# Performance work log

Hardware: AMD Instinct MI355X
Metric: run time of the kernel (lower is better)

Reference implementation:

```python
import jax, jax.numpy as jnp
import numpy as np

N = 100000      # nodes
E = 1600000     # edges
G = 256         # graphs in batch
F_IN = 100      # node_features
H = 64          # hidden_channels
L = 3           # num_conv_layers


def setup_inputs() -> dict:
    key = jax.random.key(0)
    ks = jax.random.split(key, 16)
    def w(k, shape, fan_in):
        return (jax.random.normal(k, shape, jnp.float32) / np.sqrt(fan_in)).astype(jnp.float32)
    return {
        "x": jax.random.normal(ks[0], (N, F_IN), jnp.float32),
        "edge_index": jax.random.randint(ks[1], (2, E), 0, N, dtype=jnp.int32),
        "batch": jnp.sort(jax.random.randint(ks[2], (N,), 0, G, dtype=jnp.int32)),
        "W_emb": w(ks[3], (F_IN, H), F_IN),
        "b_emb": jnp.zeros((H,), jnp.float32),
        "conv_W": w(ks[4], (L, H, H), H),
        "conv_b": jnp.zeros((L, H), jnp.float32),
        "W1": w(ks[5], (H, H), H),
        "b1": jnp.zeros((H,), jnp.float32),
        "W2": w(ks[6], (H, H // 2), H),
        "b2": jnp.zeros((H // 2,), jnp.float32),
        "W3": w(ks[7], (H // 2, 1), H // 2),
        "b3": jnp.zeros((1,), jnp.float32),
    }


def reference(x, edge_index, batch, W_emb, b_emb, conv_W, conv_b, W1, b1, W2, b2, W3, b3):
    # --- GCN normalization with self-loops (PyG GCNConv defaults) ---
    loop = jnp.arange(N, dtype=edge_index.dtype)
    src = jnp.concatenate([edge_index[0], loop])  # [E+N]
    dst = jnp.concatenate([edge_index[1], loop])  # [E+N]
    deg = jax.ops.segment_sum(jnp.ones_like(dst, jnp.float32), dst, num_segments=N)
    dinv = jax.lax.rsqrt(jnp.maximum(deg, 1.0))   # deg >= 1 because of self-loops
    norm = dinv[src] * dinv[dst]                   # [E+N]

    # --- embed ---
    h = jax.nn.relu(x @ W_emb + b_emb)             # [N, H]

    # --- stacked GCNConv: h' = scatter_add(norm * (hW)[src] -> dst) + b ---
    for i in range(conv_W.shape[0]):
        hw = h @ conv_W[i]                          # [N, H]
        msg = hw[src] * norm[:, None]               # [E+N, H] gather + scale
        agg = jax.ops.segment_sum(msg, dst, num_segments=N)
        h = jax.nn.relu(agg + conv_b[i])

    # --- global mean pool over batch ids ---
    cnt = jax.ops.segment_sum(jnp.ones((N,), jnp.float32), batch, num_segments=G)
    pooled = jax.ops.segment_sum(h, batch, num_segments=G) / jnp.maximum(cnt, 1.0)[:, None]

    # --- MLP readout 64 -> 64 -> 32 -> 1 ---
    r = jax.nn.relu(pooled @ W1 + b1)
    r = jax.nn.relu(r @ W2 + b2)
    return r @ W3 + b3                              # [G, 1]
```

## Files before the change

### kernel.cpp

```cpp
#include <hip/hip_runtime.h>
#include <hip/hip_bf16.h>

#define NN 100000
#define NE 1600000
#define NG 256
#define FIN 100
#define HH 64

#define BSHIFT 9
#define BSIZE 512
#define NBUCK ((NN + BSIZE - 1) / BSIZE)
#define BCAP 9216
#define CHUNK 4096
#define NPLACE ((NE + CHUNK - 1) / CHUNK)

#define NBLK64 ((NN + 63) / 64)
#define AGG8B ((NN + 31) / 32)

#define SXE 136
#define SH 72

typedef __attribute__((ext_vector_type(8))) short short8;
typedef __attribute__((ext_vector_type(4))) float f32x4;

__device__ __forceinline__ float relu_f(float x){ return x > 0.f ? x : 0.f; }
__device__ __forceinline__ unsigned short f2b(float f) {
    unsigned int u = __float_as_uint(f);
    u += 0x7fffu + ((u >> 16) & 1u);
    return (unsigned short)(u >> 16);
}
__device__ __forceinline__ unsigned pk2(float a, float b) {
    return (unsigned)f2b(a) | ((unsigned)f2b(b) << 16);
}
__device__ __forceinline__ float b2f(unsigned short h) {
    return __uint_as_float(((unsigned int)h) << 16);
}
__device__ __forceinline__ float lo32(unsigned u){ return __uint_as_float(u << 16); }
__device__ __forceinline__ float hi32(unsigned u){ return __uint_as_float(u & 0xffff0000u); }

__global__ __launch_bounds__(256) void k_prep(const float* __restrict__ Wemb,
                                              const float* __restrict__ convW,
                                              unsigned short* __restrict__ WeT,
                                              unsigned short* __restrict__ WcT,
                                              int* __restrict__ bucket_cnt) {
    int t = threadIdx.x;
    for (int i = t; i < NBUCK; i += 256) bucket_cnt[i] = 0;
    for (int i = t; i < 64 * 128; i += 256) WeT[i] = 0;
    __syncthreads();
    for (int i = t; i < FIN * HH; i += 256) {
        int k = i >> 6, n = i & 63;
        WeT[n * 128 + k] = f2b(Wemb[i]);
    }
    for (int l = 0; l < 3; ++l)
        for (int i = t; i < HH * HH; i += 256) {
            int k = i >> 6, n = i & 63;
            WcT[l * 4096 + n * 64 + k] = f2b(convW[l * 4096 + i]);
        }
}

__global__ __launch_bounds__(256) void k_bplace(const int* __restrict__ src,
                                                const int* __restrict__ dst,
                                                int* __restrict__ bucket_cnt,
                                                unsigned int* __restrict__ upairs) {
    __shared__ int h[NBUCK];
    __shared__ int base[NBUCK];
    int t = threadIdx.x;
    for (int i = t; i < NBUCK; i += 256) h[i] = 0;
    __syncthreads();
    int e0 = blockIdx.x * CHUNK;
    int e1 = e0 + CHUNK; if (e1 > NE) e1 = NE;
    for (int i = e0 + t; i < e1; i += 256) atomicAdd(&h[dst[i] >> BSHIFT], 1);
    __syncthreads();
    for (int i = t; i < NBUCK; i += 256) {
        int c = h[i];
        base[i] = c ? atomicAdd(&bucket_cnt[i], c) : 0;
    }
    __syncthreads();
    for (int i = t; i < NBUCK; i += 256) h[i] = 0;
    __syncthreads();
    for (int i = e0 + t; i < e1; i += 256) {
        int d = dst[i];
        int b = d >> BSHIFT;
        int pos = b * BCAP + base[b] + atomicAdd(&h[b], 1);
        upairs[pos] = ((unsigned)(d & (BSIZE - 1)) << 17) | (unsigned)src[i];
    }
}

__global__ __launch_bounds__(256) void k_csr_embed(const int* __restrict__ bucket_cnt,
                                                   const unsigned int* __restrict__ upairs,
                                                   int* __restrict__ row_start,
                                                   unsigned short* __restrict__ deg16,
                                                   float* __restrict__ dinv,
                                                   int* __restrict__ csr_src,
                                                   const float* __restrict__ x,
                                                   const unsigned short* __restrict__ WeT,
                                                   const float* __restrict__ bemb,
                                                   unsigned short* __restrict__ h0) {
    __shared__ int degl[BSIZE];
    __shared__ int curl[BSIZE];
    __shared__ int wsum8[8];
    __shared__ __align__(16) unsigned short Xl[64 * SXE];
    int t = threadIdx.x;
    int lane = t & 63, w = t >> 6;

    if (blockIdx.x < NBUCK) {
        int b = blockIdx.x;
        int nbase = b << BSHIFT;
        int ncnt = NN - nbase; if (ncnt > BSIZE) ncnt = BSIZE;
        for (int i = t; i < BSIZE; i += 256) degl[i] = 0;
        __syncthreads();
        int p0 = b * BCAP;
        int p1 = p0 + bucket_cnt[b];
        for (int i = p0 + t; i < p1; i += 256) atomicAdd(&degl[upairs[i] >> 17], 1);
        __syncthreads();
        int vals[2], incs[2];
        #pragma unroll
        for (int k = 0; k < 2; ++k) {
            int seg = w + k * 4;
            int v = degl[seg * 64 + lane];
            int inc = v;
            for (int off = 1; off < 64; off <<= 1) {
                int n = __shfl_up(inc, off, 64);
                if (lane >= off) inc += n;
            }
            vals[k] = v; incs[k] = inc;
            if (lane == 63) wsum8[seg] = inc;
        }
        __syncthreads();
        #pragma unroll
        for (int k = 0; k < 2; ++k) {
            int seg = w + k * 4;
            int soff = 0;
            for (int s = 0; s < 8; ++s) if (s < seg) soff += wsum8[s];
            int idx = seg * 64 + lane;
            int rs = p0 + soff + incs[k] - vals[k];
            curl[idx] = rs;
            if (idx < ncnt) {
                row_start[nbase + idx] = rs;
                deg16[nbase + idx] = (unsigned short)vals[k];
                dinv[nbase + idx] = rsqrtf((float)(vals[k] + 1));
            }
        }
        __syncthreads();
        for (int i = p0 + t; i < p1; i += 256) {
            unsigned pk = upairs[i];
            int pos = atomicAdd(&curl[pk >> 17], 1);
            csr_src[pos] = (int)(pk & 0x1FFFFu);
        }
        return;
    }

    int row0 = (blockIdx.x - NBUCK) * 64;
    unsigned* Xl32 = (unsigned*)Xl;
    for (int i = t; i < 64 * 25; i += 256) {
        int r = i / 25, q = i - r * 25;
        int row = row0 + r;
        uint2 pkd = {0u, 0u};
        if (row < NN) {
            float4 xv = *reinterpret_cast<const float4*>(&x[(size_t)row * FIN + q * 4]);
            pkd.x = pk2(xv.x, xv.y);
            pkd.y = pk2(xv.z, xv.w);
        }
        *reinterpret_cast<uint2*>(&Xl[r * SXE + q * 4]) = pkd;
    }
    for (int i = t; i < 64 * 18; i += 256) {
        int r = i / 18, q = i - r * 18;
        Xl32[r * 68 + 50 + q] = 0u;
    }
    __syncthreads();
    int m16 = lane & 15, g4 = lane >> 4;
    f32x4 acc[4] = {{0,0,0,0},{0,0,0,0},{0,0,0,0},{0,0,0,0}};
    const unsigned short* Arow = &Xl[(w * 16 + m16) * SXE + g4 * 8];
    #pragma unroll
    for (int kk = 0; kk < 4; ++kk) {
        short8 a = *reinterpret_cast<const short8*>(Arow + kk * 32);
        #pragma unroll
        for (int c = 0; c < 4; ++c) {
            short8 bf = *reinterpret_cast<const short8*>(&WeT[(size_t)(c * 16 + m16) * 128 + g4 * 8 + kk * 32]);
            acc[c] = __builtin_amdgcn_mfma_f32_16x16x32_bf16(a, bf, acc[c], 0, 0, 0);
        }
    }
    __syncthreads();
    unsigned short* hl = Xl;
    #pragma unroll
    for (int c = 0; c < 4; ++c) {
        int col = c * 16 + m16;
        float bb = bemb[col];
        #pragma unroll
        for (int r = 0; r < 4; ++r) {
            int rr = w * 16 + g4 * 4 + r;
            hl[rr * SH + col] = f2b(relu_f(acc[c][r] + bb));
        }
    }
    __syncthreads();
    for (int i = t; i < 64 * 8; i += 256) {
        int r = i >> 3, c8 = i & 7;
        int row = row0 + r;
        if (row < NN)
            *reinterpret_cast<uint4*>(&h0[(size_t)row * HH + c8 * 8]) =
                *reinterpret_cast<const uint4*>(&hl[r * SH + c8 * 8]);
    }
}

__global__ __launch_bounds__(256) void k_gemm(const unsigned short* __restrict__ X,
                                              const unsigned short* __restrict__ WT,
                                              const float* __restrict__ dinv,
                                              unsigned short* __restrict__ gout) {
    __shared__ __align__(16) unsigned short Xl[64 * SH];
    int t = threadIdx.x, w = t >> 6, lane = t & 63;
    int row0 = blockIdx.x * 64;
    for (int i = t; i < 64 * 8; i += 256) {
        int r = i >> 3, c8 = i & 7;
        int row = row0 + r;
        short8 v = {0,0,0,0,0,0,0,0};
        if (row < NN) v = *reinterpret_cast<const short8*>(&X[(size_t)row * HH + c8 * 8]);
        *reinterpret_cast<short8*>(&Xl[r * SH + c8 * 8]) = v;
    }
    __syncthreads();
    int m16 = lane & 15, g4 = lane >> 4;
    f32x4 acc[4] = {{0,0,0,0},{0,0,0,0},{0,0,0,0},{0,0,0,0}};
    const unsigned short* Arow = &Xl[(w * 16 + m16) * SH + g4 * 8];
    #pragma unroll
    for (int kk = 0; kk < 2; ++kk) {
        short8 a = *reinterpret_cast<const short8*>(Arow + kk * 32);
        #pragma unroll
        for (int c = 0; c < 4; ++c) {
            short8 bf = *reinterpret_cast<const short8*>(&WT[(size_t)(c * 16 + m16) * 64 + g4 * 8 + kk * 32]);
            acc[c] = __builtin_amdgcn_mfma_f32_16x16x32_bf16(a, bf, acc[c], 0, 0, 0);
        }
    }
    __syncthreads();
    float dv[4];
    #pragma unroll
    for (int r = 0; r < 4; ++r) {
        int row = row0 + w * 16 + g4 * 4 + r;
        dv[r] = (row < NN) ? dinv[row] : 0.f;
    }
    #pragma unroll
    for (int c = 0; c < 4; ++c) {
        int col = c * 16 + m16;
        #pragma unroll
        for (int r = 0; r < 4; ++r) {
            int rr = w * 16 + g4 * 4 + r;
            Xl[rr * SH + col] = f2b(dv[r] * acc[c][r]);
        }
    }
    __syncthreads();
    for (int i = t; i < 64 * 8; i += 256) {
        int r = i >> 3, c8 = i & 7;
        int row = row0 + r;
        if (row < NN)
            *reinterpret_cast<uint4*>(&gout[(size_t)row * HH + c8 * 8]) =
                *reinterpret_cast<const uint4*>(&Xl[r * SH + c8 * 8]);
    }
}

__global__ __launch_bounds__(256) void k_agg8(const int* __restrict__ row_start,
                                              const unsigned short* __restrict__ deg16,
                                              const int* __restrict__ csr_src,
                                              const unsigned short* __restrict__ g,
                                              const float* __restrict__ dinv,
                                              const float* __restrict__ bL,
                                              unsigned short* __restrict__ hout) {
    int t = threadIdx.x;
    int lane = t & 63, w = t >> 6;
    int oct = lane >> 3;
    int sub = lane & 7;
    int v = (blockIdx.x * 4 + w) * 8 + oct;
    bool valid = v < NN;
    int st = 0, n = 0;
    float a0=0.f,a1=0.f,a2=0.f,a3=0.f,a4=0.f,a5=0.f,a6=0.f,a7=0.f;
    if (valid) {
        st = row_start[v];
        n = deg16[v];
        uint4 u = *reinterpret_cast<const uint4*>(&g[(size_t)v * HH + sub * 8]);
        a0 = lo32(u.x); a1 = hi32(u.x); a2 = lo32(u.y); a3 = hi32(u.y);
        a4 = lo32(u.z); a5 = hi32(u.z); a6 = lo32(u.w); a7 = hi32(u.w);
    }
    int sb = oct << 3;
    for (int base = 0; base < n; base += 8) {
        int m = n - base; if (m > 8) m = 8;
        int sv = (sub < m) ? csr_src[st + base + sub] : 0;
        int j = 0;
        for (; j + 4 <= m; j += 4) {
            int s0 = __shfl(sv, sb + j),     s1 = __shfl(sv, sb + j + 1);
            int s2 = __shfl(sv, sb + j + 2), s3 = __shfl(sv, sb + j + 3);
            uint4 u0 = *reinterpret_cast<const uint4*>(&g[(size_t)s0 * HH + sub * 8]);
            uint4 u1 = *reinterpret_cast<const uint4*>(&g[(size_t)s1 * HH + sub * 8]);
            uint4 u2 = *reinterpret_cast<const uint4*>(&g[(size_t)s2 * HH + sub * 8]);
            uint4 u3 = *reinterpret_cast<const uint4*>(&g[(size_t)s3 * HH + sub * 8]);
            a0 += lo32(u0.x); a1 += hi32(u0.x); a2 += lo32(u0.y); a3 += hi32(u0.y);
            a4 += lo32(u0.z); a5 += hi32(u0.z); a6 += lo32(u0.w); a7 += hi32(u0.w);
            a0 += lo32(u1.x); a1 += hi32(u1.x); a2 += lo32(u1.y); a3 += hi32(u1.y);
            a4 += lo32(u1.z); a5 += hi32(u1.z); a6 += lo32(u1.w); a7 += hi32(u1.w);
            a0 += lo32(u2.x); a1 += hi32(u2.x); a2 += lo32(u2.y); a3 += hi32(u2.y);
            a4 += lo32(u2.z); a5 += hi32(u2.z); a6 += lo32(u2.w); a7 += hi32(u2.w);
            a0 += lo32(u3.x); a1 += hi32(u3.x); a2 += lo32(u3.y); a3 += hi32(u3.y);
            a4 += lo32(u3.z); a5 += hi32(u3.z); a6 += lo32(u3.w); a7 += hi32(u3.w);
        }
        for (; j < m; ++j) {
            int s = __shfl(sv, sb + j);
            uint4 u = *reinterpret_cast<const uint4*>(&g[(size_t)s * HH + sub * 8]);
            a0 += lo32(u.x); a1 += hi32(u.x); a2 += lo32(u.y); a3 += hi32(u.y);
            a4 += lo32(u.z); a5 += hi32(u.z); a6 += lo32(u.w); a7 += hi32(u.w);
        }
    }
    if (valid) {
        float4 bb0 = *reinterpret_cast<const float4*>(&bL[sub * 8]);
        float4 bb1 = *reinterpret_cast<const float4*>(&bL[sub * 8 + 4]);
        float dv = dinv[v];
        uint4 outv;
        outv.x = pk2(relu_f(dv * a0 + bb0.x), relu_f(dv * a1 + bb0.y));
        outv.y = pk2(relu_f(dv * a2 + bb0.z), relu_f(dv * a3 + bb0.w));
        outv.z = pk2(relu_f(dv * a4 + bb1.x), relu_f(dv * a5 + bb1.y));
        outv.w = pk2(relu_f(dv * a6 + bb1.z), relu_f(dv * a7 + bb1.w));
        *reinterpret_cast<uint4*>(&hout[(size_t)v * HH + sub * 8]) = outv;
    }
}

__global__ __launch_bounds__(512) void k_pool_mlp(const unsigned short* __restrict__ h,
                                                  const int* __restrict__ batch,
                                                  const float* __restrict__ W1, const float* __restrict__ b1,
                                                  const float* __restrict__ W2, const float* __restrict__ b2,
                                                  const float* __restrict__ W3, const float* __restrict__ b3,
                                                  float* __restrict__ out) {
    int g = blockIdx.x;
    int lo = 0, hi_s = NN;
    while (lo < hi_s) { int mid = (lo + hi_s) >> 1; if (batch[mid] < g) lo = mid + 1; else hi_s = mid; }
    int lo2 = lo, hi = NN;
    while (lo2 < hi) { int mid = (lo2 + hi) >> 1; if (batch[mid] < g + 1) lo2 = mid + 1; else hi = mid; }
    int lane = threadIdx.x & 63;
    int wave = threadIdx.x >> 6;
    float s = 0.f;
    for (int n = lo + wave; n < hi; n += 8) {
        s += b2f(h[(size_t)n * HH + lane]);
    }
    __shared__ float red[8][64];
    __shared__ float pv[64];
    __shared__ float tv[64];
    __shared__ float qv[32];
    red[wave][lane] = s;
    __syncthreads();
    int cnt = hi - lo;
    float invc = 1.f / (float)(cnt > 0 ? cnt : 1);
    if (threadIdx.x < 64) {
        float acc = 0.f;
        #pragma unroll
        for (int r = 0; r < 8; ++r) acc += red[r][lane];
        pv[lane] = acc * invc;
    }
    __syncthreads();
    if (threadIdx.x < 64) {
        int j = threadIdx.x;
        float s1 = b1[j];
        #pragma unroll
        for (int k = 0; k < 64; ++k) s1 = fmaf(pv[k], W1[k * 64 + j], s1);
        tv[j] = relu_f(s1);
    }
    __syncthreads();
    if (threadIdx.x < 32) {
        int j = threadIdx.x;
        float s2 = b2[j];
        #pragma unroll
        for (int k = 0; k < 64; ++k) s2 = fmaf(tv[k], W2[k * 32 + j], s2);
        qv[j] = relu_f(s2);
    }
    __syncthreads();
    if (threadIdx.x == 0) {
        float s3 = b3[0];
        #pragma unroll
        for (int k = 0; k < 32; ++k) s3 = fmaf(qv[k], W3[k], s3);
        out[g] = s3;
    }
}

extern "C" void kernel_launch(void* const* d_in, const int* in_sizes, int n_in,
                              void* d_out, int out_size, void* d_ws, size_t ws_size,
                              hipStream_t stream) {
    const float* x    = (const float*)d_in[0];
    const int*   ei   = (const int*)d_in[1];
    const int*   batch= (const int*)d_in[2];
    const float* Wemb = (const float*)d_in[3];
    const float* bemb = (const float*)d_in[4];
    const float* convW= (const float*)d_in[5];
    const float* convb= (const float*)d_in[6];
    const float* W1   = (const float*)d_in[7];
    const float* b1   = (const float*)d_in[8];
    const float* W2   = (const float*)d_in[9];
    const float* b2   = (const float*)d_in[10];
    const float* W3   = (const float*)d_in[11];
    const float* b3   = (const float*)d_in[12];
    float* out = (float*)d_out;

    auto alignup = [](size_t v) { return (v + 255) & ~(size_t)255; };
    char* p = (char*)d_ws;
    int*   row_start    = (int*)p;            p += alignup((size_t)NN * 4);
    unsigned short* deg16 = (unsigned short*)p; p += alignup((size_t)NN * 2);
    float* dinv         = (float*)p;          p += alignup((size_t)NN * 4);
    int*   bucket_cnt   = (int*)p;            p += alignup((size_t)NBUCK * 4);
    int*   csr_src      = (int*)p;            p += alignup((size_t)NBUCK * BCAP * 4);
    unsigned short* WeT = (unsigned short*)p; p += alignup((size_t)64 * 128 * 2);
    unsigned short* WcT = (unsigned short*)p; p += alignup((size_t)3 * 4096 * 2);
    unsigned short* hbuf = (unsigned short*)p; p += alignup((size_t)NN * HH * 2);
    unsigned short* gbuf = (unsigned short*)p; p += alignup((size_t)NN * HH * 2);
    unsigned int* upairs = (unsigned int*)gbuf;

    const int* srcA = ei;
    const int* dstA = ei + NE;

    k_prep<<<1, 256, 0, stream>>>(Wemb, convW, WeT, WcT, bucket_cnt);
    k_bplace<<<NPLACE, 256, 0, stream>>>(srcA, dstA, bucket_cnt, upairs);

    k_csr_embed<<<NBUCK + NBLK64, 256, 0, stream>>>(bucket_cnt, upairs, row_start, deg16, dinv,
                                                    csr_src, x, WeT, bemb, hbuf);

    k_gemm<<<NBLK64, 256, 0, stream>>>(hbuf, WcT + 0 * 4096, dinv, gbuf);
    k_agg8<<<AGG8B, 256, 0, stream>>>(row_start, deg16, csr_src, gbuf, dinv, convb + 0 * HH, hbuf);
    k_gemm<<<NBLK64, 256, 0, stream>>>(hbuf, WcT + 1 * 4096, dinv, gbuf);
    k_agg8<<<AGG8B, 256, 0, stream>>>(row_start, deg16, csr_src, gbuf, dinv, convb + 1 * HH, hbuf);
    k_gemm<<<NBLK64, 256, 0, stream>>>(hbuf, WcT + 2 * 4096, dinv, gbuf);
    k_agg8<<<AGG8B, 256, 0, stream>>>(row_start, deg16, csr_src, gbuf, dinv, convb + 2 * HH, hbuf);

    k_pool_mlp<<<NG, 512, 0, stream>>>(hbuf, batch, W1, b1, W2, b2, W3, b3, out);
}
```

Baseline: 247.0 us.

## Fuse conv GEMMs into embed and aggregation kernels, shrink CSR buckets

Removes the standalone k_gemm launches by folding the first layer's dense transform into the embed kernel and the following layers' transforms into the tail of each aggregation kernel. The first aggregation applies source-side dinv scaling per edge because the embed output is left unscaled. Bucket size drops from 512 to 256 nodes so the CSR build launches more, smaller blocks. This saves three launches and two full read/write passes over the N×64 feature buffer, at the cost of extra syncs and shared-memory traffic in the aggregation kernel and a per-edge dinv gather in layer one.

```diff
diff --git a/kernel.cpp b/kernel.cpp
--- a/kernel.cpp
+++ b/kernel.cpp
@@ -7,15 +7,15 @@
 #define FIN 100
 #define HH 64
 
-#define BSHIFT 9
-#define BSIZE 512
+#define BSHIFT 8
+#define BSIZE 256
 #define NBUCK ((NN + BSIZE - 1) / BSIZE)
-#define BCAP 9216
+#define BCAP 4608
 #define CHUNK 4096
 #define NPLACE ((NE + CHUNK - 1) / CHUNK)
 
 #define NBLK64 ((NN + 63) / 64)
-#define AGG8B ((NN + 31) / 32)
+#define AGGB (NN / 32)
 
 #define SXE 136
 #define SH 72
@@ -95,10 +95,11 @@
                                                    const float* __restrict__ x,
                                                    const unsigned short* __restrict__ WeT,
                                                    const float* __restrict__ bemb,
-                                                   unsigned short* __restrict__ h0) {
+                                                   const unsigned short* __restrict__ W0T,
+                                                   unsigned short* __restrict__ g0) {
     __shared__ int degl[BSIZE];
     __shared__ int curl[BSIZE];
-    __shared__ int wsum8[8];
+    __shared__ int wsum4[4];
     __shared__ __align__(16) unsigned short Xl[64 * SXE];
     int t = threadIdx.x;
     int lane = t & 63, w = t >> 6;
@@ -113,33 +114,23 @@
         int p1 = p0 + bucket_cnt[b];
         for (int i = p0 + t; i < p1; i += 256) atomicAdd(&degl[upairs[i] >> 17], 1);
         __syncthreads();
-        int vals[2], incs[2];
-        #pragma unroll
-        for (int k = 0; k < 2; ++k) {
-            int seg = w + k * 4;
-            int v = degl[seg * 64 + lane];
-            int inc = v;
-            for (int off = 1; off < 64; off <<= 1) {
-                int n = __shfl_up(inc, off, 64);
-                if (lane >= off) inc += n;
-            }
-            vals[k] = v; incs[k] = inc;
-            if (lane == 63) wsum8[seg] = inc;
-        }
+        int vseg = degl[w * 64 + lane];
+        int inc = vseg;
+        for (int off = 1; off < 64; off <<= 1) {
+            int n = __shfl_up(inc, off, 64);
+            if (lane >= off) inc += n;
+        }
+        if (lane == 63) wsum4[w] = inc;
         __syncthreads();
-        #pragma unroll
-        for (int k = 0; k < 2; ++k) {
-            int seg = w + k * 4;
-            int soff = 0;
-            for (int s = 0; s < 8; ++s) if (s < seg) soff += wsum8[s];
-            int idx = seg * 64 + lane;
-            int rs = p0 + soff + incs[k] - vals[k];
-            curl[idx] = rs;
-            if (idx < ncnt) {
-                row_start[nbase + idx] = rs;
-                deg16[nbase + idx] = (unsigned short)vals[k];
-                dinv[nbase + idx] = rsqrtf((float)(vals[k] + 1));
-            }
+        int soff = 0;
+        for (int s = 0; s < w; ++s) soff += wsum4[s];
+        int idx = w * 64 + lane;
+        int rs = p0 + soff + inc - vseg;
+        curl[idx] = rs;
+        if (idx < ncnt) {
+            row_start[nbase + idx] = rs;
+            deg16[nbase + idx] = (unsigned short)vseg;
+            dinv[nbase + idx] = rsqrtf((float)(vseg + 1));
         }
         __syncthreads();
         for (int i = p0 + t; i < p1; i += 256) {
@@ -193,94 +184,69 @@
         }
     }
     __syncthreads();
+    f32x4 acc2[4] = {{0,0,0,0},{0,0,0,0},{0,0,0,0},{0,0,0,0}};
+    const unsigned short* Hrow = &hl[(w * 16 + m16) * SH + g4 * 8];
+    #pragma unroll
+    for (int kk = 0; kk < 2; ++kk) {
+        short8 a = *reinterpret_cast<const short8*>(Hrow + kk * 32);
+        #pragma unroll
+        for (int c = 0; c < 4; ++c) {
+            short8 bf = *reinterpret_cast<const short8*>(&W0T[(size_t)(c * 16 + m16) * 64 + g4 * 8 + kk * 32]);
+            acc2[c] = __builtin_amdgcn_mfma_f32_16x16x32_bf16(a, bf, acc2[c], 0, 0, 0);
+        }
+    }
+    __syncthreads();
+    #pragma unroll
+    for (int c = 0; c < 4; ++c) {
+        int col = c * 16 + m16;
+        #pragma unroll
+        for (int r = 0; r < 4; ++r) {
+            int rr = w * 16 + g4 * 4 + r;
+            hl[rr * SH + col] = f2b(acc2[c][r]);
+        }
+    }
+    __syncthreads();
     for (int i = t; i < 64 * 8; i += 256) {
         int r = i >> 3, c8 = i & 7;
         int row = row0 + r;
         if (row < NN)
-            *reinterpret_cast<uint4*>(&h0[(size_t)row * HH + c8 * 8]) =
-                *reinterpret_cast<const uint4*>(&hl[r * SH + c8 * 8]);
-    }
-}
-
-__global__ __launch_bounds__(256) void k_gemm(const unsigned short* __restrict__ X,
-                                              const unsigned short* __restrict__ WT,
-                                              const float* __restrict__ dinv,
-                                              unsigned short* __restrict__ gout) {
-    __shared__ __align__(16) unsigned short Xl[64 * SH];
-    int t = threadIdx.x, w = t >> 6, lane = t & 63;
-    int row0 = blockIdx.x * 64;
-    for (int i = t; i < 64 * 8; i += 256) {
-        int r = i >> 3, c8 = i & 7;
-        int row = row0 + r;
-        short8 v = {0,0,0,0,0,0,0,0};
-        if (row < NN) v = *reinterpret_cast<const short8*>(&X[(size_t)row * HH + c8 * 8]);
-        *reinterpret_cast<short8*>(&Xl[r * SH + c8 * 8]) = v;
-    }
-    __syncthreads();
-    int m16 = lane & 15, g4 = lane >> 4;
-    f32x4 acc[4] = {{0,0,0,0},{0,0,0,0},{0,0,0,0},{0,0,0,0}};
-    const unsigned short* Arow = &Xl[(w * 16 + m16) * SH + g4 * 8];
-    #pragma unroll
-    for (int kk = 0; kk < 2; ++kk) {
-        short8 a = *reinterpret_cast<const short8*>(Arow + kk * 32);
-        #pragma unroll
-        for (int c = 0; c < 4; ++c) {
-            short8 bf = *reinterpret_cast<const short8*>(&WT[(size_t)(c * 16 + m16) * 64 + g4 * 8 + kk * 32]);
-            acc[c] = __builtin_amdgcn_mfma_f32_16x16x32_bf16(a, bf, acc[c], 0, 0, 0);
-        }
-    }
-    __syncthreads();
-    float dv[4];
-    #pragma unroll
-    for (int r = 0; r < 4; ++r) {
-        int row = row0 + w * 16 + g4 * 4 + r;
-        dv[r] = (row < NN) ? dinv[row] : 0.f;
-    }
-    #pragma unroll
-    for (int c = 0; c < 4; ++c) {
-        int col = c * 16 + m16;
-        #pragma unroll
-        for (int r = 0; r < 4; ++r) {
-            int rr = w * 16 + g4 * 4 + r;
-            Xl[rr * SH + col] = f2b(dv[r] * acc[c][r]);
-        }
-    }
-    __syncthreads();
-    for (int i = t; i < 64 * 8; i += 256) {
-        int r = i >> 3, c8 = i & 7;
-        int row = row0 + r;
-        if (row < NN)
-            *reinterpret_cast<uint4*>(&gout[(size_t)row * HH + c8 * 8]) =
+            *reinterpret_cast<uint4*>(&g0[(size_t)row * HH + c8 * 8]) =
                 *reinterpret_cast<const uint4*>(&Xl[r * SH + c8 * 8]);
     }
 }
 
-__global__ __launch_bounds__(256) void k_agg8(const int* __restrict__ row_start,
-                                              const unsigned short* __restrict__ deg16,
-                                              const int* __restrict__ csr_src,
-                                              const unsigned short* __restrict__ g,
-                                              const float* __restrict__ dinv,
-                                              const float* __restrict__ bL,
-                                              unsigned short* __restrict__ hout) {
+template <int ES, int GEMM>
+__global__ __launch_bounds__(256) void k_agg(const int* __restrict__ row_start,
+                                             const unsigned short* __restrict__ deg16,
+                                             const int* __restrict__ csr_src,
+                                             const unsigned short* __restrict__ g,
+                                             const float* __restrict__ dinv,
+                                             const float* __restrict__ bL,
+                                             const unsigned short* __restrict__ WT,
+                                             unsigned short* __restrict__ outbuf) {
+    __shared__ __align__(16) unsigned short hl[32 * SH];
     int t = threadIdx.x;
     int lane = t & 63, w = t >> 6;
     int oct = lane >> 3;
     int sub = lane & 7;
-    int v = (blockIdx.x * 4 + w) * 8 + oct;
-    bool valid = v < NN;
-    int st = 0, n = 0;
-    float a0=0.f,a1=0.f,a2=0.f,a3=0.f,a4=0.f,a5=0.f,a6=0.f,a7=0.f;
-    if (valid) {
-        st = row_start[v];
-        n = deg16[v];
+    int v0 = blockIdx.x * 32;
+    int v = v0 + w * 8 + oct;
+    int st = row_start[v];
+    int n = deg16[v];
+    float dvv = dinv[v];
+    float a0,a1,a2,a3,a4,a5,a6,a7;
+    {
         uint4 u = *reinterpret_cast<const uint4*>(&g[(size_t)v * HH + sub * 8]);
-        a0 = lo32(u.x); a1 = hi32(u.x); a2 = lo32(u.y); a3 = hi32(u.y);
-        a4 = lo32(u.z); a5 = hi32(u.z); a6 = lo32(u.w); a7 = hi32(u.w);
+        float sc = ES ? dvv : 1.f;
+        a0 = sc*lo32(u.x); a1 = sc*hi32(u.x); a2 = sc*lo32(u.y); a3 = sc*hi32(u.y);
+        a4 = sc*lo32(u.z); a5 = sc*hi32(u.z); a6 = sc*lo32(u.w); a7 = sc*hi32(u.w);
     }
     int sb = oct << 3;
     for (int base = 0; base < n; base += 8) {
         int m = n - base; if (m > 8) m = 8;
         int sv = (sub < m) ? csr_src[st + base + sub] : 0;
+        float dl = 0.f;
+        if (ES) dl = (sub < m) ? dinv[sv] : 0.f;
         int j = 0;
         for (; j + 4 <= m; j += 4) {
             int s0 = __shfl(sv, sb + j),     s1 = __shfl(sv, sb + j + 1);
@@ -289,32 +255,93 @@
             uint4 u1 = *reinterpret_cast<const uint4*>(&g[(size_t)s1 * HH + sub * 8]);
             uint4 u2 = *reinterpret_cast<const uint4*>(&g[(size_t)s2 * HH + sub * 8]);
             uint4 u3 = *reinterpret_cast<const uint4*>(&g[(size_t)s3 * HH + sub * 8]);
-            a0 += lo32(u0.x); a1 += hi32(u0.x); a2 += lo32(u0.y); a3 += hi32(u0.y);
-            a4 += lo32(u0.z); a5 += hi32(u0.z); a6 += lo32(u0.w); a7 += hi32(u0.w);
-            a0 += lo32(u1.x); a1 += hi32(u1.x); a2 += lo32(u1.y); a3 += hi32(u1.y);
-            a4 += lo32(u1.z); a5 += hi32(u1.z); a6 += lo32(u1.w); a7 += hi32(u1.w);
-            a0 += lo32(u2.x); a1 += hi32(u2.x); a2 += lo32(u2.y); a3 += hi32(u2.y);
-            a4 += lo32(u2.z); a5 += hi32(u2.z); a6 += lo32(u2.w); a7 += hi32(u2.w);
-            a0 += lo32(u3.x); a1 += hi32(u3.x); a2 += lo32(u3.y); a3 += hi32(u3.y);
-            a4 += lo32(u3.z); a5 += hi32(u3.z); a6 += lo32(u3.w); a7 += hi32(u3.w);
+            if (ES) {
+                float d0 = __shfl(dl, sb + j),     d1 = __shfl(dl, sb + j + 1);
+                float d2 = __shfl(dl, sb + j + 2), d3 = __shfl(dl, sb + j + 3);
+                a0 = fmaf(d0, lo32(u0.x), a0); a1 = fmaf(d0, hi32(u0.x), a1);
+                a2 = fmaf(d0, lo32(u0.y), a2); a3 = fmaf(d0, hi32(u0.y), a3);
+                a4 = fmaf(d0, lo32(u0.z), a4); a5 = fmaf(d0, hi32(u0.z), a5);
+                a6 = fmaf(d0, lo32(u0.w), a6); a7 = fmaf(d0, hi32(u0.w), a7);
+                a0 = fmaf(d1, lo32(u1.x), a0); a1 = fmaf(d1, hi32(u1.x), a1);
+                a2 = fmaf(d1, lo32(u1.y), a2); a3 = fmaf(d1, hi32(u1.y), a3);
+                a4 = fmaf(d1, lo32(u1.z), a4); a5 = fmaf(d1, hi32(u1.z), a5);
+                a6 = fmaf(d1, lo32(u1.w), a6); a7 = fmaf(d1, hi32(u1.w), a7);
+                a0 = fmaf(d2, lo32(u2.x), a0); a1 = fmaf(d2, hi32(u2.x), a1);
+                a2 = fmaf(d2, lo32(u2.y), a2); a3 = fmaf(d2, hi32(u2.y), a3);
+                a4 = fmaf(d2, lo32(u2.z), a4); a5 = fmaf(d2, hi32(u2.z), a5);
+                a6 = fmaf(d2, lo32(u2.w), a6); a7 = fmaf(d2, hi32(u2.w), a7);
+                a0 = fmaf(d3, lo32(u3.x), a0); a1 = fmaf(d3, hi32(u3.x), a1);
+                a2 = fmaf(d3, lo32(u3.y), a2); a3 = fmaf(d3, hi32(u3.y), a3);
+                a4 = fmaf(d3, lo32(u3.z), a4); a5 = fmaf(d3, hi32(u3.z), a5);
+                a6 = fmaf(d3, lo32(u3.w), a6); a7 = fmaf(d3, hi32(u3.w), a7);
+            } else {
+                a0 += lo32(u0.x); a1 += hi32(u0.x); a2 += lo32(u0.y); a3 += hi32(u0.y);
+                a4 += lo32(u0.z); a5 += hi32(u0.z); a6 += lo32(u0.w); a7 += hi32(u0.w);
+                a0 += lo32(u1.x); a1 += hi32(u1.x); a2 += lo32(u1.y); a3 += hi32(u1.y);
+                a4 += lo32(u1.z); a5 += hi32(u1.z); a6 += lo32(u1.w); a7 += hi32(u1.w);
+                a0 += lo32(u2.x); a1 += hi32(u2.x); a2 += lo32(u2.y); a3 += hi32(u2.y);
+                a4 += lo32(u2.z); a5 += hi32(u2.z); a6 += lo32(u2.w); a7 += hi32(u2.w);
+                a0 += lo32(u3.x); a1 += hi32(u3.x); a2 += lo32(u3.y); a3 += hi32(u3.y);
+                a4 += lo32(u3.z); a5 += hi32(u3.z); a6 += lo32(u3.w); a7 += hi32(u3.w);
+            }
         }
         for (; j < m; ++j) {
             int s = __shfl(sv, sb + j);
             uint4 u = *reinterpret_cast<const uint4*>(&g[(size_t)s * HH + sub * 8]);
-            a0 += lo32(u.x); a1 += hi32(u.x); a2 += lo32(u.y); a3 += hi32(u.y);
-            a4 += lo32(u.z); a5 += hi32(u.z); a6 += lo32(u.w); a7 += hi32(u.w);
-        }
-    }
-    if (valid) {
-        float4 bb0 = *reinterpret_cast<const float4*>(&bL[sub * 8]);
-        float4 bb1 = *reinterpret_cast<const float4*>(&bL[sub * 8 + 4]);
-        float dv = dinv[v];
-        uint4 outv;
-        outv.x = pk2(relu_f(dv * a0 + bb0.x), relu_f(dv * a1 + bb0.y));
-        outv.y = pk2(relu_f(dv * a2 + bb0.z), relu_f(dv * a3 + bb0.w));
-        outv.z = pk2(relu_f(dv * a4 + bb1.x), relu_f(dv * a5 + bb1.y));
-        outv.w = pk2(relu_f(dv * a6 + bb1.z), relu_f(dv * a7 + bb1.w));
-        *reinterpret_cast<uint4*>(&hout[(size_t)v * HH + sub * 8]) = outv;
+            if (ES) {
+                float d = __shfl(dl, sb + j);
+                a0 = fmaf(d, lo32(u.x), a0); a1 = fmaf(d, hi32(u.x), a1);
+                a2 = fmaf(d, lo32(u.y), a2); a3 = fmaf(d, hi32(u.y), a3);
+                a4 = fmaf(d, lo32(u.z), a4); a5 = fmaf(d, hi32(u.z), a5);
+                a6 = fmaf(d, lo32(u.w), a6); a7 = fmaf(d, hi32(u.w), a7);
+            } else {
+                a0 += lo32(u.x); a1 += hi32(u.x); a2 += lo32(u.y); a3 += hi32(u.y);
+                a4 += lo32(u.z); a5 += hi32(u.z); a6 += lo32(u.w); a7 += hi32(u.w);
+            }
+        }
+    }
+    float4 bb0 = *reinterpret_cast<const float4*>(&bL[sub * 8]);
+    float4 bb1 = *reinterpret_cast<const float4*>(&bL[sub * 8 + 4]);
+    uint4 hv;
+    hv.x = pk2(relu_f(dvv * a0 + bb0.x), relu_f(dvv * a1 + bb0.y));
+    hv.y = pk2(relu_f(dvv * a2 + bb0.z), relu_f(dvv * a3 + bb0.w));
+    hv.z = pk2(relu_f(dvv * a4 + bb1.x), relu_f(dvv * a5 + bb1.y));
+    hv.w = pk2(relu_f(dvv * a6 + bb1.z), relu_f(dvv * a7 + bb1.w));
+    if (!GEMM) {
+        *reinterpret_cast<uint4*>(&outbuf[(size_t)v * HH + sub * 8]) = hv;
+        return;
+    }
+    int lrow = w * 8 + oct;
+    *reinterpret_cast<uint4*>(&hl[lrow * SH + sub * 8]) = hv;
+    __syncthreads();
+    int m16 = lane & 15, g4 = lane >> 4;
+    int rb = w & 1, cbase = (w >> 1) * 2;
+    f32x4 acc2[2] = {{0,0,0,0},{0,0,0,0}};
+    #pragma unroll
+    for (int kk = 0; kk < 2; ++kk) {
+        short8 a = *reinterpret_cast<const short8*>(&hl[(rb * 16 + m16) * SH + g4 * 8 + kk * 32]);
+        #pragma unroll
+        for (int c = 0; c < 2; ++c) {
+            short8 bf = *reinterpret_cast<const short8*>(&WT[(size_t)((cbase + c) * 16 + m16) * 64 + g4 * 8 + kk * 32]);
+            acc2[c] = __builtin_amdgcn_mfma_f32_16x16x32_bf16(a, bf, acc2[c], 0, 0, 0);
+        }
+    }
+    __syncthreads();
+    #pragma unroll
+    for (int r = 0; r < 4; ++r) {
+        int lr = rb * 16 + g4 * 4 + r;
+        float dv2 = dinv[v0 + lr];
+        #pragma unroll
+        for (int c = 0; c < 2; ++c) {
+            int col = (cbase + c) * 16 + m16;
+            hl[lr * SH + col] = f2b(dv2 * acc2[c][r]);
+        }
+    }
+    __syncthreads();
+    {
+        int r = t >> 3, c8 = t & 7;
+        *reinterpret_cast<uint4*>(&outbuf[(size_t)(v0 + r) * HH + c8 * 8]) =
+            *reinterpret_cast<const uint4*>(&hl[r * SH + c8 * 8]);
     }
 }
 
@@ -401,9 +428,9 @@
     int*   csr_src      = (int*)p;            p += alignup((size_t)NBUCK * BCAP * 4);
     unsigned short* WeT = (unsigned short*)p; p += alignup((size_t)64 * 128 * 2);
     unsigned short* WcT = (unsigned short*)p; p += alignup((size_t)3 * 4096 * 2);
-    unsigned short* hbuf = (unsigned short*)p; p += alignup((size_t)NN * HH * 2);
-    unsigned short* gbuf = (unsigned short*)p; p += alignup((size_t)NN * HH * 2);
-    unsigned int* upairs = (unsigned int*)gbuf;
+    unsigned short* bufA = (unsigned short*)p; p += alignup((size_t)NN * HH * 2);
+    unsigned short* bufB = (unsigned short*)p; p += alignup((size_t)NN * HH * 2);
+    unsigned int* upairs = (unsigned int*)bufB;
 
     const int* srcA = ei;
     const int* dstA = ei + NE;
@@ -412,14 +439,14 @@
     k_bplace<<<NPLACE, 256, 0, stream>>>(srcA, dstA, bucket_cnt, upairs);
 
     k_csr_embed<<<NBUCK + NBLK64, 256, 0, stream>>>(bucket_cnt, upairs, row_start, deg16, dinv,
-                                                    csr_src, x, WeT, bemb, hbuf);
-
-    k_gemm<<<NBLK64, 256, 0, stream>>>(hbuf, WcT + 0 * 4096, dinv, gbuf);
-    k_agg8<<<AGG8B, 256, 0, stream>>>(row_start, deg16, csr_src, gbuf, dinv, convb + 0 * HH, hbuf);
-    k_gemm<<<NBLK64, 256, 0, stream>>>(hbuf, WcT + 1 * 4096, dinv, gbuf);
-    k_agg8<<<AGG8B, 256, 0, stream>>>(row_start, deg16, csr_src, gbuf, dinv, convb + 1 * HH, hbuf);
-    k_gemm<<<NBLK64, 256, 0, stream>>>(hbuf, WcT + 2 * 4096, dinv, gbuf);
-    k_agg8<<<AGG8B, 256, 0, stream>>>(row_start, deg16, csr_src, gbuf, dinv, convb + 2 * HH, hbuf);
-
-    k_pool_mlp<<<NG, 512, 0, stream>>>(hbuf, batch, W1, b1, W2, b2, W3, b3, out);
-}
+                                                    csr_src, x, WeT, bemb, WcT + 0 * 4096, bufA);
+
+    k_agg<1,1><<<AGGB, 256, 0, stream>>>(row_start, deg16, csr_src, bufA, dinv,
+                                         convb + 0 * HH, WcT + 1 * 4096, bufB);
+    k_agg<0,1><<<AGGB, 256, 0, stream>>>(row_start, deg16, csr_src, bufB, dinv,
+                                         convb + 1 * HH, WcT + 2 * 4096, bufA);
+    k_agg<0,0><<<AGGB, 256, 0, stream>>>(row_start, deg16, csr_src, bufA, dinv,
+                                         convb + 2 * HH, nullptr, bufB);
+
+    k_pool_mlp<<<NG, 512, 0, stream>>>(bufB, batch, W1, b1, W2, b2, W3, b3, out);
+}
```

Measured after the change: 217.7 us. 11.8% less time.
